# Kernel optimization log

Hardware: AMD Instinct MI355X
Metric: run time of the kernel (lower is better)

The kernel has to match this reference:

```python
import jax, jax.numpy as jnp
import numpy as np

N_NODES = 100000
N_EDGES = 1600000
NFEAT, NHID, NCLASS = 512, 256, 40
ALPHA = 1.0
N_POWERS = 10


def setup_inputs() -> dict:
    key = jax.random.key(0)
    ks = jax.random.split(key, 8)
    x = jax.random.normal(ks[0], (N_NODES, NFEAT), dtype=jnp.float32)
    edge_index = jax.random.randint(ks[1], (2, N_EDGES), 0, N_NODES)
    # Kaiming-ish init, scale = 1/sqrt(fan_in)
    W1 = jax.random.normal(ks[2], (NHID, NFEAT), dtype=jnp.float32) / np.sqrt(NFEAT)
    b1 = jnp.zeros((NHID,), jnp.float32)
    W2 = jax.random.normal(ks[3], (NHID, NHID), dtype=jnp.float32) / np.sqrt(NHID)
    b2 = jnp.zeros((NHID,), jnp.float32)
    W3 = jax.random.normal(ks[4], (NCLASS, NHID), dtype=jnp.float32) / np.sqrt(NHID)
    b3 = jnp.zeros((NCLASS,), jnp.float32)
    return {"x": x, "edge_index": edge_index, "W1": W1, "b1": b1,
            "W2": W2, "b2": b2, "W3": W3, "b3": b3}


def reference(x, edge_index, W1, b1, W2, b2, W3, b3):
    N = x.shape[0]
    # --- build DA-normalized adjacency with self-loops (to_normalized_sparsetensor, mode='DA') ---
    self_loop = jnp.arange(N)
    rows = jnp.concatenate([edge_index[0], self_loop])  # [E+N]
    cols = jnp.concatenate([edge_index[1], self_loop])  # [E+N]
    deg = jax.ops.segment_sum(jnp.ones(rows.shape[0], x.dtype), rows, num_segments=N)
    # DA mode: rows scaled by deg_inv_sqrt^2 == deg^{-1}
    deg_inv = jnp.where(deg > 0, 1.0 / deg, 0.0)
    w = deg_inv[rows]  # per-edge weight, [E+N]

    def spmm(v):  # A @ v, v: [N, C]
        return jax.ops.segment_sum(w[:, None] * v[cols], rows, num_segments=N)

    # --- MLP (dropout=0, eval mode) ---
    h = jax.nn.relu(x @ W1.T + b1)
    h = jax.nn.relu(h @ W2.T + b2)
    h = h @ W3.T + b3  # [N, NCLASS]

    # --- approximate_invphi_x power iteration (beta=0 branch) ---
    c1 = ALPHA / (1.0 + ALPHA)
    c2 = 1.0 / (1.0 + ALPHA)
    invphi = h
    for _ in range(N_POWERS):
        invphi = c1 * spmm(invphi) + c2 * h
    return invphi
```

## Files before the change

kernel.cpp:

```cpp
#include <hip/hip_runtime.h>
#include <type_traits>

#define N_NODES 100000
#define N_EDGES 1600000
#define NFEAT 512
#define NHID 256
#define NCLASS 40
#define NPAD 100096
#define NPAD2 100352

#define NBUCK 196
#define BROWS 512
#define NBLK_BIN 256
#define EPB 6250

#define CDUM 1916000
#define COLN 1916032

#define ZA (N_NODES * 32)
#define ZB (N_NODES * 8)
#define BLK_A 1563
#define BLK_B 391

typedef __bf16 bf16;
typedef __bf16 bf16x8 __attribute__((ext_vector_type(8)));
typedef __bf16 bf16x4 __attribute__((ext_vector_type(4)));
typedef float f32x4 __attribute__((ext_vector_type(4)));
typedef int i32x4 __attribute__((ext_vector_type(4)));


__global__ __launch_bounds__(256) void bin_count(const int* __restrict__ rows,
                                                 int* __restrict__ bcnt) {
    __shared__ int hist[NBUCK];
    int t = threadIdx.x, b = blockIdx.x;
    for (int i = t; i < NBUCK; i += 256) hist[i] = 0;
    __syncthreads();
    int base = b * EPB;
    for (int i = t; i < EPB; i += 256) atomicAdd(&hist[rows[base + i] >> 9], 1);
    __syncthreads();
    for (int i = t; i < NBUCK; i += 256) bcnt[i * NBLK_BIN + b] = hist[i];
}

__global__ __launch_bounds__(256) void bin_scan(const int* __restrict__ bcnt,
                                                int* __restrict__ boff2,
                                                int* __restrict__ btot) {
    __shared__ int sh[256];
    int t = threadIdx.x, bu = blockIdx.x;
    int v = bcnt[bu * 256 + t];
    sh[t] = v;
    __syncthreads();
    for (int off = 1; off < 256; off <<= 1) {
        int x = (t >= off) ? sh[t - off] : 0;
        __syncthreads();
        sh[t] += x;
        __syncthreads();
    }
    boff2[t * NBUCK + bu] = sh[t] - v;
    if (t == 255) btot[bu] = sh[255];
}

__global__ __launch_bounds__(256) void base_scan(const int* __restrict__ btot,
                                                 int* __restrict__ bbase) {
    __shared__ int sh[256];
    int t = threadIdx.x;
    int v = (t < NBUCK) ? btot[t] : 0;
    sh[t] = v;
    __syncthreads();
    for (int off = 1; off < 256; off <<= 1) {
        int x = (t >= off) ? sh[t - off] : 0;
        __syncthreads();
        sh[t] += x;
        __syncthreads();
    }
    if (t < NBUCK) bbase[t] = sh[t] - v;
    if (t == NBUCK - 1) bbase[NBUCK] = sh[t];
}

__global__ __launch_bounds__(256) void bin_scatter(const int* __restrict__ rows,
                                                   const int* __restrict__ cols,
                                                   const int* __restrict__ boff2,
                                                   const int* __restrict__ bbase,
                                                   int* __restrict__ binned) {
    __shared__ int cur[NBUCK];
    int t = threadIdx.x, b = blockIdx.x;
    for (int i = t; i < NBUCK; i += 256) cur[i] = bbase[i] + boff2[b * NBUCK + i];
    __syncthreads();
    int base = b * EPB;
    for (int i = t; i < EPB; i += 256) {
        int r = rows[base + i], c = cols[base + i];
        int pos = atomicAdd(&cur[r >> 9], 1);
        binned[pos] = ((r & 511) << 17) | c;
    }
}

__global__ __launch_bounds__(256) void bucket_csr(const int* __restrict__ binned,
                                                  const int* __restrict__ bbase,
                                                  int2* __restrict__ rowptr2,
                                                  int* __restrict__ colidx,
                                                  float* __restrict__ dinv) {
    __shared__ int cnt[BROWS];
    __shared__ int pref[BROWS];
    __shared__ int psum[256];
    int t = threadIdx.x, bu = blockIdx.x;
    cnt[t] = 0;
    cnt[t + 256] = 0;
    __syncthreads();
    int base = bbase[bu], end = bbase[bu + 1];
    for (int i = base + t; i < end; i += 256) atomicAdd(&cnt[binned[i] >> 17], 1);
    __syncthreads();
    int c0 = cnt[2 * t], c1 = cnt[2 * t + 1];
    int p0 = (c0 + 3) & ~3, p1 = (c1 + 3) & ~3;
    psum[t] = p0 + p1;
    __syncthreads();
    for (int off = 1; off < 256; off <<= 1) {
        int x = (t >= off) ? psum[t - off] : 0;
        __syncthreads();
        psum[t] += x;
        __syncthreads();
    }
    int pex = psum[t] - (p0 + p1);
    pref[2 * t] = pex;
    pref[2 * t + 1] = pex + p0;
    __syncthreads();
    int pbase = (base & ~3) + bu * 1600;
#pragma unroll
    for (int j = 0; j < 2; j++) {
        int idx = t + j * 256;
        int grow = bu * BROWS + idx;
        int rc = cnt[idx];
        int st = pbase + pref[idx];
        int en = st + ((rc + 3) & ~3);
        if (grow < N_NODES) {
            rowptr2[grow] = make_int2(st, en);
            dinv[grow] = 0.5f / (float)(rc + 1);
            for (int k = st + rc; k < en; k++) colidx[k] = N_NODES;
        } else {
            rowptr2[grow] = make_int2(0, 0);
        }
        pref[idx] = st;
    }
    __syncthreads();
    for (int i = base + t; i < end; i += 256) {
        int v = binned[i];
        int pos = atomicAdd(&pref[v >> 17], 1);
        colidx[pos] = v & 0x1FFFF;
    }
}


__global__ void cvt_f2b(const float* __restrict__ a, bf16* __restrict__ b, int n) {
    int i = blockIdx.x * 256 + threadIdx.x;
    if (i < n) b[i] = (bf16)a[i];
}

__global__ void pad_w3(const float* __restrict__ W3, const float* __restrict__ b3,
                       bf16* __restrict__ W3p, float* __restrict__ b3p) {
    int i = blockIdx.x * 256 + threadIdx.x;
    int r = i >> 8;
    W3p[i] = (bf16)((r < NCLASS) ? W3[(size_t)r * 256 + (i & 255)] : 0.f);
    if (i < 64) b3p[i] = (i < NCLASS) ? b3[i] : 0.f;
}

__global__ void zero_dummy(bf16* vAi, bf16* vA0, bf16* vA1,
                           bf16* vBi, bf16* vB0, bf16* vB1,
                           int* colidx) {
    int i = threadIdx.x;
    if (i < 32) {
        vAi[(size_t)ZA + i] = (bf16)0.f;
        vA0[(size_t)ZA + i] = (bf16)0.f;
        vA1[(size_t)ZA + i] = (bf16)0.f;
    }
    if (i < 8) {
        vBi[(size_t)ZB + i] = (bf16)0.f;
        vB0[(size_t)ZB + i] = (bf16)0.f;
        vB1[(size_t)ZB + i] = (bf16)0.f;
        colidx[CDUM + i] = N_NODES;
    }
}


template <int BN, typename AT, bool RELU, int OUTMODE>
__global__ __launch_bounds__(256) void gemm_mfma(const AT* __restrict__ A,
                                                 const bf16* __restrict__ B,
                                                 const float* __restrict__ bias,
                                                 bf16* __restrict__ Cb,
                                                 float* __restrict__ hA,
                                                 float* __restrict__ hB,
                                                 bf16* __restrict__ vA0,
                                                 bf16* __restrict__ vB0,
                                                 int M, int K, int Nout) {
    constexpr int LDT = 40;
    constexpr int WTM = (BN == 128) ? 64 : 32;
    constexpr int MI = WTM / 16;
    constexpr int WMC = 128 / WTM;
    constexpr int BG = BN / 64;
    constexpr bool AF32 = std::is_same<AT, float>::value;
    __shared__ bf16 As[2][128 * LDT];
    __shared__ bf16 Bs[2][BN * LDT];

    int tid = threadIdx.x;
    int wave = tid >> 6, lane = tid & 63;
    int waveM = wave % WMC, waveN = wave / WMC;
    int lc = lane & 15, lq = lane >> 4;

    f32x4 acc[MI][4];
#pragma unroll
    for (int i = 0; i < MI; i++)
#pragma unroll
        for (int j = 0; j < 4; j++) acc[i][j] = (f32x4){0.f, 0.f, 0.f, 0.f};

    int sr = tid >> 2;
    int sc = (tid & 3) * 8;

    float4 paE[2][2], paO[2][2];
    bf16x8 baE[2], baO[2];
    bf16x8 bbE[BG], bbO[BG];

    auto LOAD = [&](int k0, float4 (&pa)[2][2], bf16x8 (&ba)[2], bf16x8 (&bb)[BG]) {
#pragma unroll
        for (int g = 0; g < 2; g++) {
            int grow = blockIdx.y * 128 + sr + g * 64;
            if constexpr (AF32) {
                if (grow < M) {
                    const float* ap = A + (size_t)grow * K + k0 + sc;
                    pa[g][0] = *(const float4*)ap;
                    pa[g][1] = *(const float4*)(ap + 4);
                } else {
                    pa[g][0] = (float4){0.f, 0.f, 0.f, 0.f};
                    pa[g][1] = (float4){0.f, 0.f, 0.f, 0.f};
                }
            } else {
                ba[g] = (grow < M) ? *(const bf16x8*)(A + (size_t)grow * K + k0 + sc)
                                   : (bf16x8){};
            }
        }
#pragma unroll
        for (int g = 0; g < BG; g++) {
            int brow = blockIdx.x * BN + sr + g * 64;
            bb[g] = *(const bf16x8*)(B + (size_t)brow * K + k0 + sc);
        }
    };
    auto STORE = [&](int buf, float4 (&pa)[2][2], bf16x8 (&ba)[2], bf16x8 (&bb)[BG]) {
#pragma unroll
        for (int g = 0; g < 2; g++) {
            bf16x8 val;
            if constexpr (AF32) {
                val[0] = (bf16)pa[g][0].x; val[1] = (bf16)pa[g][0].y;
                val[2] = (bf16)pa[g][0].z; val[3] = (bf16)pa[g][0].w;
                val[4] = (bf16)pa[g][1].x; val[5] = (bf16)pa[g][1].y;
                val[6] = (bf16)pa[g][1].z; val[7] = (bf16)pa[g][1].w;
            } else {
                val = ba[g];
            }
            *(bf16x8*)&As[buf][(sr + g * 64) * LDT + sc] = val;
        }
#pragma unroll
        for (int g = 0; g < BG; g++)
            *(bf16x8*)&Bs[buf][(sr + g * 64) * LDT + sc] = bb[g];
    };
    auto COMPUTE = [&](int cb) {
        bf16x8 af[MI], bfr[4];
#pragma unroll
        for (int i = 0; i < MI; i++)
            af[i] = *(const bf16x8*)&As[cb][(waveM * WTM + i * 16 + lc) * LDT + lq * 8];
#pragma unroll
        for (int j = 0; j < 4; j++)
            bfr[j] = *(const bf16x8*)&Bs[cb][(waveN * 64 + j * 16 + lc) * LDT + lq * 8];
#pragma unroll
        for (int i = 0; i < MI; i++)
#pragma unroll
            for (int j = 0; j < 4; j++)
                acc[i][j] = __builtin_amdgcn_mfma_f32_16x16x32_bf16(af[i], bfr[j], acc[i][j], 0, 0, 0);
    };

    int nt = K / 32;
    LOAD(0, paE, baE, bbE);
    STORE(0, paE, baE, bbE);
    LOAD(32, paE, baE, bbE);
    LOAD(64, paO, baO, bbO);
    __syncthreads();
    for (int t = 0; t < nt; t += 2) {
        STORE(1, paE, baE, bbE);
        if (t + 3 < nt) LOAD((t + 3) * 32, paE, baE, bbE);
        COMPUTE(0);
        __syncthreads();
        if (t + 2 < nt) STORE(0, paO, baO, bbO);
        if (t + 4 < nt) LOAD((t + 4) * 32, paO, baO, bbO);
        COMPUTE(1);
        __syncthreads();
    }

#pragma unroll
    for (int i = 0; i < MI; i++) {
        int row0 = blockIdx.y * 128 + waveM * WTM + i * 16 + lq * 4;
#pragma unroll
        for (int j = 0; j < 4; j++) {
            int colL = waveN * 64 + j * 16 + lc;
            int col = blockIdx.x * BN + colL;
            float bv = bias[col];
#pragma unroll
            for (int reg = 0; reg < 4; reg++) {
                int rr = row0 + reg;
                if (rr < M) {
                    float v = acc[i][j][reg] + bv;
                    if (RELU) v = v > 0.f ? v : 0.f;
                    if (OUTMODE == 0) {
                        Cb[(size_t)rr * Nout + col] = (bf16)v;
                    } else {
                        if (col < 32) {
                            hA[(size_t)rr * 32 + col] = 0.5f * v;
                            vA0[(size_t)rr * 32 + col] = (bf16)v;
                        } else if (col < NCLASS) {
                            hB[(size_t)rr * 8 + (col - 32)] = 0.5f * v;
                            vB0[(size_t)rr * 8 + (col - 32)] = (bf16)v;
                        }
                    }
                }
            }
        }
    }
}


__global__ __launch_bounds__(256) void spmm_split(const bf16* __restrict__ vA,
                                                  const bf16* __restrict__ vB,
                                                  const float* __restrict__ hA,
                                                  const float* __restrict__ hB,
                                                  const int2* __restrict__ rowptr2,
                                                  const int* __restrict__ colidx,
                                                  const float* __restrict__ dinv,
                                                  bf16* __restrict__ oA,
                                                  bf16* __restrict__ oB,
                                                  float* __restrict__ outF,
                                                  int final_it) {
    int b = blockIdx.x;
    int lane = threadIdx.x & 63;
    const int* cdum = colidx + CDUM;
    if (b < BLK_A) {
        int w = b * 4 + (threadIdx.x >> 6);
        int sub = lane & 3;
        int r = w * 16 + (lane >> 2);
        if (r >= N_NODES) return;
        int2 se = rowptr2[r];
        int sx = se.x, d = se.y - se.x;
        int m = d;
#pragma unroll
        for (int off = 4; off < 64; off <<= 1) {
            int x = __shfl_xor(m, off);
            m = m > x ? m : x;
        }
        float4 hv0 = *(const float4*)(hA + (size_t)r * 32 + sub * 8);
        float4 hv1 = *(const float4*)(hA + (size_t)r * 32 + sub * 8 + 4);
        float dv = dinv[r];
        bf16x8 sv = *(const bf16x8*)(vA + (size_t)r * 32 + sub * 8);
        float a[8];
#pragma unroll
        for (int k = 0; k < 8; k++) a[k] = (float)sv[k];
        i32x4 cc = *(const i32x4*)(d > 0 ? colidx + sx : cdum);
        i32x4 cn = *(const i32x4*)(4 < d ? colidx + sx + 4 : cdum);
        bf16x8 G0 = *(const bf16x8*)(vA + (size_t)cc[0] * 32 + sub * 8);
        bf16x8 G1 = *(const bf16x8*)(vA + (size_t)cc[1] * 32 + sub * 8);
        bf16x8 G2 = *(const bf16x8*)(vA + (size_t)cc[2] * 32 + sub * 8);
        bf16x8 G3 = *(const bf16x8*)(vA + (size_t)cc[3] * 32 + sub * 8);
        int m8 = (m + 7) & ~7;
        for (int i = 0; i < m8; i += 8) {
            i32x4 ci8 = *(const i32x4*)((i + 8 < d) ? colidx + sx + i + 8 : cdum);
            bf16x8 H0 = *(const bf16x8*)(vA + (size_t)cn[0] * 32 + sub * 8);
            bf16x8 H1 = *(const bf16x8*)(vA + (size_t)cn[1] * 32 + sub * 8);
            bf16x8 H2 = *(const bf16x8*)(vA + (size_t)cn[2] * 32 + sub * 8);
            bf16x8 H3 = *(const bf16x8*)(vA + (size_t)cn[3] * 32 + sub * 8);
#pragma unroll
            for (int k = 0; k < 8; k++)
                a[k] += ((float)G0[k] + (float)G1[k]) + ((float)G2[k] + (float)G3[k]);
            cn = *(const i32x4*)((i + 12 < d) ? colidx + sx + i + 12 : cdum);
            G0 = *(const bf16x8*)(vA + (size_t)ci8[0] * 32 + sub * 8);
            G1 = *(const bf16x8*)(vA + (size_t)ci8[1] * 32 + sub * 8);
            G2 = *(const bf16x8*)(vA + (size_t)ci8[2] * 32 + sub * 8);
            G3 = *(const bf16x8*)(vA + (size_t)ci8[3] * 32 + sub * 8);
#pragma unroll
            for (int k = 0; k < 8; k++)
                a[k] += ((float)H0[k] + (float)H1[k]) + ((float)H2[k] + (float)H3[k]);
        }
        float res[8];
        res[0] = dv * a[0] + hv0.x; res[1] = dv * a[1] + hv0.y;
        res[2] = dv * a[2] + hv0.z; res[3] = dv * a[3] + hv0.w;
        res[4] = dv * a[4] + hv1.x; res[5] = dv * a[5] + hv1.y;
        res[6] = dv * a[6] + hv1.z; res[7] = dv * a[7] + hv1.w;
        if (final_it) {
            *(float4*)(outF + (size_t)r * NCLASS + sub * 8) = (float4){res[0], res[1], res[2], res[3]};
            *(float4*)(outF + (size_t)r * NCLASS + sub * 8 + 4) = (float4){res[4], res[5], res[6], res[7]};
        } else {
            bf16x8 o;
#pragma unroll
            for (int k = 0; k < 8; k++) o[k] = (bf16)res[k];
            *(bf16x8*)(oA + (size_t)r * 32 + sub * 8) = o;
        }
    } else {
        int w = (b - BLK_A) * 4 + (threadIdx.x >> 6);
        int r = w * 64 + lane;
        int rz = (r < N_NODES) ? r : 0;
        int2 se = rowptr2[r];
        int sx = se.x, d = se.y - se.x;
        int m = d;
#pragma unroll
        for (int off = 1; off < 64; off <<= 1) {
            int x = __shfl_xor(m, off);
            m = m > x ? m : x;
        }
        float4 h0 = *(const float4*)(hB + (size_t)rz * 8);
        float4 h1 = *(const float4*)(hB + (size_t)rz * 8 + 4);
        float dv = dinv[rz];
        bf16x8 sv = *(const bf16x8*)(vB + (size_t)rz * 8);
        float a[8];
#pragma unroll
        for (int k = 0; k < 8; k++) a[k] = (float)sv[k];
        i32x4 cc = *(const i32x4*)(d > 0 ? colidx + sx : cdum);
        i32x4 cn = *(const i32x4*)(4 < d ? colidx + sx + 4 : cdum);
        bf16x8 G0 = *(const bf16x8*)(vB + (size_t)cc[0] * 8);
        bf16x8 G1 = *(const bf16x8*)(vB + (size_t)cc[1] * 8);
        bf16x8 G2 = *(const bf16x8*)(vB + (size_t)cc[2] * 8);
        bf16x8 G3 = *(const bf16x8*)(vB + (size_t)cc[3] * 8);
        int m8 = (m + 7) & ~7;
        for (int i = 0; i < m8; i += 8) {
            i32x4 ci8 = *(const i32x4*)((i + 8 < d) ? colidx + sx + i + 8 : cdum);
            bf16x8 H0 = *(const bf16x8*)(vB + (size_t)cn[0] * 8);
            bf16x8 H1 = *(const bf16x8*)(vB + (size_t)cn[1] * 8);
            bf16x8 H2 = *(const bf16x8*)(vB + (size_t)cn[2] * 8);
            bf16x8 H3 = *(const bf16x8*)(vB + (size_t)cn[3] * 8);
#pragma unroll
            for (int k = 0; k < 8; k++)
                a[k] += ((float)G0[k] + (float)G1[k]) + ((float)G2[k] + (float)G3[k]);
            cn = *(const i32x4*)((i + 12 < d) ? colidx + sx + i + 12 : cdum);
            G0 = *(const bf16x8*)(vB + (size_t)ci8[0] * 8);
            G1 = *(const bf16x8*)(vB + (size_t)ci8[1] * 8);
            G2 = *(const bf16x8*)(vB + (size_t)ci8[2] * 8);
            G3 = *(const bf16x8*)(vB + (size_t)ci8[3] * 8);
#pragma unroll
            for (int k = 0; k < 8; k++)
                a[k] += ((float)H0[k] + (float)H1[k]) + ((float)H2[k] + (float)H3[k]);
        }
        if (r < N_NODES) {
            float res[8];
            res[0] = dv * a[0] + h0.x; res[1] = dv * a[1] + h0.y;
            res[2] = dv * a[2] + h0.z; res[3] = dv * a[3] + h0.w;
            res[4] = dv * a[4] + h1.x; res[5] = dv * a[5] + h1.y;
            res[6] = dv * a[6] + h1.z; res[7] = dv * a[7] + h1.w;
            if (final_it) {
                *(float4*)(outF + (size_t)r * NCLASS + 32) = (float4){res[0], res[1], res[2], res[3]};
                *(float4*)(outF + (size_t)r * NCLASS + 36) = (float4){res[4], res[5], res[6], res[7]};
            } else {
                bf16x8 o;
#pragma unroll
                for (int k = 0; k < 8; k++) o[k] = (bf16)res[k];
                *(bf16x8*)(oB + (size_t)r * 8) = o;
            }
        }
    }
}


extern "C" void kernel_launch(void* const* d_in, const int* in_sizes, int n_in,
                              void* d_out, int out_size, void* d_ws, size_t ws_size,
                              hipStream_t stream) {
    const float* x  = (const float*)d_in[0];
    const int*   ei = (const int*)d_in[1];
    const float* W1 = (const float*)d_in[2];
    const float* b1 = (const float*)d_in[3];
    const float* W2 = (const float*)d_in[4];
    const float* b2 = (const float*)d_in[5];
    const float* W3 = (const float*)d_in[6];
    const float* b3 = (const float*)d_in[7];
    float* out = (float*)d_out;
    const int* rows = ei;
    const int* cols = ei + N_EDGES;

    char* p = (char*)d_ws;
    bf16* hid1 = (bf16*)p;                 p += (size_t)N_NODES * NHID * 2;
    bf16* hid2 = (bf16*)p;                 p += (size_t)N_NODES * NHID * 2;
    float* hA  = (float*)p;                p += (size_t)N_NODES * 32 * 4;
    float* hB  = (float*)p;                p += (size_t)N_NODES * 8 * 4;
    bf16* vAi  = (bf16*)p;                 p += (size_t)(N_NODES + 1) * 32 * 2;
    bf16* vA0  = (bf16*)p;                 p += (size_t)(N_NODES + 1) * 32 * 2;
    bf16* vA1  = (bf16*)p;                 p += (size_t)(N_NODES + 1) * 32 * 2;
    bf16* vBi  = (bf16*)p;                 p += (size_t)(N_NODES + 1) * 8 * 2;
    bf16* vB0  = (bf16*)p;                 p += (size_t)(N_NODES + 1) * 8 * 2;
    bf16* vB1  = (bf16*)p;                 p += (size_t)(N_NODES + 1) * 8 * 2;
    bf16* W1b  = (bf16*)p;                 p += (size_t)NHID * NFEAT * 2;
    bf16* W2b  = (bf16*)p;                 p += (size_t)NHID * NHID * 2;
    bf16* W3p  = (bf16*)p;                 p += (size_t)64 * NHID * 2;
    float* b3p = (float*)p;                p += 64 * 4;
    int* bcnt    = (int*)p;                p += (size_t)NPAD * 4;
    int2* rowptr2 = (int2*)p;              p += (size_t)NPAD2 * 8;
    int* boff2   = (int*)p;                p += (size_t)N_NODES * 4;
    int* colidx  = (int*)p;                p += (size_t)COLN * 4;
    int* bsum    = (int*)p;                p += 512 * 4;
    float* dinv  = (float*)p;              p += (size_t)N_NODES * 4;

    int* btot  = bsum;
    int* bbase = bsum + 256;
    int* binned = (int*)hid1;

    bin_count<<<NBLK_BIN, 256, 0, stream>>>(rows, bcnt);
    bin_scan<<<NBUCK, 256, 0, stream>>>(bcnt, boff2, btot);
    base_scan<<<1, 256, 0, stream>>>(btot, bbase);
    bin_scatter<<<NBLK_BIN, 256, 0, stream>>>(rows, cols, boff2, bbase, binned);
    bucket_csr<<<NBUCK, 256, 0, stream>>>(binned, bbase, rowptr2, colidx, dinv);

    cvt_f2b<<<(NHID * NFEAT + 255) / 256, 256, 0, stream>>>(W1, W1b, NHID * NFEAT);
    cvt_f2b<<<(NHID * NHID + 255) / 256, 256, 0, stream>>>(W2, W2b, NHID * NHID);
    pad_w3<<<(64 * NHID) / 256, 256, 0, stream>>>(W3, b3, W3p, b3p);

    {
        int M = N_NODES;
        int gy = (M + 127) / 128;
        gemm_mfma<128, float, true, 0><<<dim3(2, gy), 256, 0, stream>>>(
            x, W1b, b1, hid1, nullptr, nullptr, nullptr, nullptr, M, NFEAT, NHID);
        gemm_mfma<128, bf16, true, 0><<<dim3(2, gy), 256, 0, stream>>>(
            hid1, W2b, b2, hid2, nullptr, nullptr, nullptr, nullptr, M, NHID, NHID);
        gemm_mfma<64, bf16, false, 1><<<dim3(1, gy), 256, 0, stream>>>(
            hid2, W3p, b3p, nullptr, hA, hB, vAi, vBi, M, NHID, 64);
    }

    zero_dummy<<<1, 64, 0, stream>>>(vAi, vA0, vA1, vBi, vB0, vB1, colidx);

    const bf16* sA = vAi;
    const bf16* sB = vBi;
    for (int it = 0; it < 10; it++) {
        int fin = (it == 9);
        bf16* dA = (it & 1) ? vA1 : vA0;
        bf16* dB = (it & 1) ? vB1 : vB0;
        spmm_split<<<BLK_A + BLK_B, 256, 0, stream>>>(
            sA, sB, hA, hB, rowptr2, colidx, dinv, dA, dB, out, fin);
        sA = dA;
        sB = dB;
    }
}
```

Measured before the change: 805.0 us.

## Split SpMM into separate column-group kernels and relax GEMM barriers and bounds checks

The fused SpMM kernel, which handled both the 32-column and 8-column feature slices in one launch, is split into two kernels. All ten iterations of the A slice now run before all ten of the B slice, so each sequence gathers from a smaller working set that can stay resident in cache. In the GEMM, the full __syncthreads is replaced by a barrier that waits only on LDS traffic, so global prefetch loads stay in flight across the barrier. Row bounds checks become a clamp to the last row. The split doubles the number of kernel launches and gives up running both slices concurrently within one launch.

```diff
diff --git a/kernel.cpp b/kernel.cpp
--- a/kernel.cpp
+++ b/kernel.cpp
@@ -27,6 +27,11 @@
 typedef __bf16 bf16x4 __attribute__((ext_vector_type(4)));
 typedef float f32x4 __attribute__((ext_vector_type(4)));
 typedef int i32x4 __attribute__((ext_vector_type(4)));
+
+__device__ __forceinline__ void barrier_keep_vmem() {
+    asm volatile("s_waitcnt lgkmcnt(0)" ::: "memory");
+    __builtin_amdgcn_s_barrier();
+}
 
 
 __global__ __launch_bounds__(256) void bin_count(const int* __restrict__ rows,
@@ -220,18 +225,13 @@
 #pragma unroll
         for (int g = 0; g < 2; g++) {
             int grow = blockIdx.y * 128 + sr + g * 64;
+            if (grow > M - 1) grow = M - 1;
             if constexpr (AF32) {
-                if (grow < M) {
-                    const float* ap = A + (size_t)grow * K + k0 + sc;
-                    pa[g][0] = *(const float4*)ap;
-                    pa[g][1] = *(const float4*)(ap + 4);
-                } else {
-                    pa[g][0] = (float4){0.f, 0.f, 0.f, 0.f};
-                    pa[g][1] = (float4){0.f, 0.f, 0.f, 0.f};
-                }
+                const float* ap = A + (size_t)grow * K + k0 + sc;
+                pa[g][0] = *(const float4*)ap;
+                pa[g][1] = *(const float4*)(ap + 4);
             } else {
-                ba[g] = (grow < M) ? *(const bf16x8*)(A + (size_t)grow * K + k0 + sc)
-                                   : (bf16x8){};
+                ba[g] = *(const bf16x8*)(A + (size_t)grow * K + k0 + sc);
             }
         }
 #pragma unroll
@@ -278,16 +278,16 @@
     STORE(0, paE, baE, bbE);
     LOAD(32, paE, baE, bbE);
     LOAD(64, paO, baO, bbO);
-    __syncthreads();
+    barrier_keep_vmem();
     for (int t = 0; t < nt; t += 2) {
         STORE(1, paE, baE, bbE);
         if (t + 3 < nt) LOAD((t + 3) * 32, paE, baE, bbE);
         COMPUTE(0);
-        __syncthreads();
+        barrier_keep_vmem();
         if (t + 2 < nt) STORE(0, paO, baO, bbO);
         if (t + 4 < nt) LOAD((t + 4) * 32, paO, baO, bbO);
         COMPUTE(1);
-        __syncthreads();
+        barrier_keep_vmem();
     }
 
 #pragma unroll
@@ -322,138 +322,143 @@
 }
 
 
-__global__ __launch_bounds__(256) void spmm_split(const bf16* __restrict__ vA,
-                                                  const bf16* __restrict__ vB,
-                                                  const float* __restrict__ hA,
-                                                  const float* __restrict__ hB,
-                                                  const int2* __restrict__ rowptr2,
-                                                  const int* __restrict__ colidx,
-                                                  const float* __restrict__ dinv,
-                                                  bf16* __restrict__ oA,
-                                                  bf16* __restrict__ oB,
-                                                  float* __restrict__ outF,
-                                                  int final_it) {
-    int b = blockIdx.x;
+__global__ __launch_bounds__(256) void spmm_A(const bf16* __restrict__ vA,
+                                              const float* __restrict__ hA,
+                                              const int2* __restrict__ rowptr2,
+                                              const int* __restrict__ colidx,
+                                              const float* __restrict__ dinv,
+                                              bf16* __restrict__ oA,
+                                              float* __restrict__ outF,
+                                              int final_it) {
     int lane = threadIdx.x & 63;
     const int* cdum = colidx + CDUM;
-    if (b < BLK_A) {
-        int w = b * 4 + (threadIdx.x >> 6);
-        int sub = lane & 3;
-        int r = w * 16 + (lane >> 2);
-        if (r >= N_NODES) return;
-        int2 se = rowptr2[r];
-        int sx = se.x, d = se.y - se.x;
-        int m = d;
-#pragma unroll
-        for (int off = 4; off < 64; off <<= 1) {
-            int x = __shfl_xor(m, off);
-            m = m > x ? m : x;
-        }
-        float4 hv0 = *(const float4*)(hA + (size_t)r * 32 + sub * 8);
-        float4 hv1 = *(const float4*)(hA + (size_t)r * 32 + sub * 8 + 4);
-        float dv = dinv[r];
-        bf16x8 sv = *(const bf16x8*)(vA + (size_t)r * 32 + sub * 8);
-        float a[8];
-#pragma unroll
-        for (int k = 0; k < 8; k++) a[k] = (float)sv[k];
-        i32x4 cc = *(const i32x4*)(d > 0 ? colidx + sx : cdum);
-        i32x4 cn = *(const i32x4*)(4 < d ? colidx + sx + 4 : cdum);
-        bf16x8 G0 = *(const bf16x8*)(vA + (size_t)cc[0] * 32 + sub * 8);
-        bf16x8 G1 = *(const bf16x8*)(vA + (size_t)cc[1] * 32 + sub * 8);
-        bf16x8 G2 = *(const bf16x8*)(vA + (size_t)cc[2] * 32 + sub * 8);
-        bf16x8 G3 = *(const bf16x8*)(vA + (size_t)cc[3] * 32 + sub * 8);
-        int m8 = (m + 7) & ~7;
-        for (int i = 0; i < m8; i += 8) {
-            i32x4 ci8 = *(const i32x4*)((i + 8 < d) ? colidx + sx + i + 8 : cdum);
-            bf16x8 H0 = *(const bf16x8*)(vA + (size_t)cn[0] * 32 + sub * 8);
-            bf16x8 H1 = *(const bf16x8*)(vA + (size_t)cn[1] * 32 + sub * 8);
-            bf16x8 H2 = *(const bf16x8*)(vA + (size_t)cn[2] * 32 + sub * 8);
-            bf16x8 H3 = *(const bf16x8*)(vA + (size_t)cn[3] * 32 + sub * 8);
-#pragma unroll
-            for (int k = 0; k < 8; k++)
-                a[k] += ((float)G0[k] + (float)G1[k]) + ((float)G2[k] + (float)G3[k]);
-            cn = *(const i32x4*)((i + 12 < d) ? colidx + sx + i + 12 : cdum);
-            G0 = *(const bf16x8*)(vA + (size_t)ci8[0] * 32 + sub * 8);
-            G1 = *(const bf16x8*)(vA + (size_t)ci8[1] * 32 + sub * 8);
-            G2 = *(const bf16x8*)(vA + (size_t)ci8[2] * 32 + sub * 8);
-            G3 = *(const bf16x8*)(vA + (size_t)ci8[3] * 32 + sub * 8);
-#pragma unroll
-            for (int k = 0; k < 8; k++)
-                a[k] += ((float)H0[k] + (float)H1[k]) + ((float)H2[k] + (float)H3[k]);
-        }
+    int w = blockIdx.x * 4 + (threadIdx.x >> 6);
+    int sub = lane & 3;
+    int r = w * 16 + (lane >> 2);
+    if (r >= N_NODES) return;
+    int2 se = rowptr2[r];
+    int sx = se.x, d = se.y - se.x;
+    int m = d;
+#pragma unroll
+    for (int off = 4; off < 64; off <<= 1) {
+        int x = __shfl_xor(m, off);
+        m = m > x ? m : x;
+    }
+    float4 hv0 = *(const float4*)(hA + (size_t)r * 32 + sub * 8);
+    float4 hv1 = *(const float4*)(hA + (size_t)r * 32 + sub * 8 + 4);
+    float dv = dinv[r];
+    bf16x8 sv = *(const bf16x8*)(vA + (size_t)r * 32 + sub * 8);
+    float a[8];
+#pragma unroll
+    for (int k = 0; k < 8; k++) a[k] = (float)sv[k];
+    i32x4 cc = *(const i32x4*)(d > 0 ? colidx + sx : cdum);
+    i32x4 cn = *(const i32x4*)(4 < d ? colidx + sx + 4 : cdum);
+    bf16x8 G0 = *(const bf16x8*)(vA + (size_t)cc[0] * 32 + sub * 8);
+    bf16x8 G1 = *(const bf16x8*)(vA + (size_t)cc[1] * 32 + sub * 8);
+    bf16x8 G2 = *(const bf16x8*)(vA + (size_t)cc[2] * 32 + sub * 8);
+    bf16x8 G3 = *(const bf16x8*)(vA + (size_t)cc[3] * 32 + sub * 8);
+    int m8 = (m + 7) & ~7;
+    for (int i = 0; i < m8; i += 8) {
+        i32x4 ci8 = *(const i32x4*)((i + 8 < d) ? colidx + sx + i + 8 : cdum);
+        bf16x8 H0 = *(const bf16x8*)(vA + (size_t)cn[0] * 32 + sub * 8);
+        bf16x8 H1 = *(const bf16x8*)(vA + (size_t)cn[1] * 32 + sub * 8);
+        bf16x8 H2 = *(const bf16x8*)(vA + (size_t)cn[2] * 32 + sub * 8);
+        bf16x8 H3 = *(const bf16x8*)(vA + (size_t)cn[3] * 32 + sub * 8);
+#pragma unroll
+        for (int k = 0; k < 8; k++)
+            a[k] += ((float)G0[k] + (float)G1[k]) + ((float)G2[k] + (float)G3[k]);
+        cn = *(const i32x4*)((i + 12 < d) ? colidx + sx + i + 12 : cdum);
+        G0 = *(const bf16x8*)(vA + (size_t)ci8[0] * 32 + sub * 8);
+        G1 = *(const bf16x8*)(vA + (size_t)ci8[1] * 32 + sub * 8);
+        G2 = *(const bf16x8*)(vA + (size_t)ci8[2] * 32 + sub * 8);
+        G3 = *(const bf16x8*)(vA + (size_t)ci8[3] * 32 + sub * 8);
+#pragma unroll
+        for (int k = 0; k < 8; k++)
+            a[k] += ((float)H0[k] + (float)H1[k]) + ((float)H2[k] + (float)H3[k]);
+    }
+    float res[8];
+    res[0] = dv * a[0] + hv0.x; res[1] = dv * a[1] + hv0.y;
+    res[2] = dv * a[2] + hv0.z; res[3] = dv * a[3] + hv0.w;
+    res[4] = dv * a[4] + hv1.x; res[5] = dv * a[5] + hv1.y;
+    res[6] = dv * a[6] + hv1.z; res[7] = dv * a[7] + hv1.w;
+    if (final_it) {
+        *(float4*)(outF + (size_t)r * NCLASS + sub * 8) = (float4){res[0], res[1], res[2], res[3]};
+        *(float4*)(outF + (size_t)r * NCLASS + sub * 8 + 4) = (float4){res[4], res[5], res[6], res[7]};
+    } else {
+        bf16x8 o;
+#pragma unroll
+        for (int k = 0; k < 8; k++) o[k] = (bf16)res[k];
+        *(bf16x8*)(oA + (size_t)r * 32 + sub * 8) = o;
+    }
+}
+
+__global__ __launch_bounds__(256) void spmm_B(const bf16* __restrict__ vB,
+                                              const float* __restrict__ hB,
+                                              const int2* __restrict__ rowptr2,
+                                              const int* __restrict__ colidx,
+                                              const float* __restrict__ dinv,
+                                              bf16* __restrict__ oB,
+                                              float* __restrict__ outF,
+                                              int final_it) {
+    int lane = threadIdx.x & 63;
+    const int* cdum = colidx + CDUM;
+    int w = blockIdx.x * 4 + (threadIdx.x >> 6);
+    int r = w * 64 + lane;
+    int rz = (r < N_NODES) ? r : 0;
+    int2 se = rowptr2[r];
+    int sx = se.x, d = se.y - se.x;
+    int m = d;
+#pragma unroll
+    for (int off = 1; off < 64; off <<= 1) {
+        int x = __shfl_xor(m, off);
+        m = m > x ? m : x;
+    }
+    float4 h0 = *(const float4*)(hB + (size_t)rz * 8);
+    float4 h1 = *(const float4*)(hB + (size_t)rz * 8 + 4);
+    float dv = dinv[rz];
+    bf16x8 sv = *(const bf16x8*)(vB + (size_t)rz * 8);
+    float a[8];
+#pragma unroll
+    for (int k = 0; k < 8; k++) a[k] = (float)sv[k];
+    i32x4 cc = *(const i32x4*)(d > 0 ? colidx + sx : cdum);
+    i32x4 cn = *(const i32x4*)(4 < d ? colidx + sx + 4 : cdum);
+    bf16x8 G0 = *(const bf16x8*)(vB + (size_t)cc[0] * 8);
+    bf16x8 G1 = *(const bf16x8*)(vB + (size_t)cc[1] * 8);
+    bf16x8 G2 = *(const bf16x8*)(vB + (size_t)cc[2] * 8);
+    bf16x8 G3 = *(const bf16x8*)(vB + (size_t)cc[3] * 8);
+    int m8 = (m + 7) & ~7;
+    for (int i = 0; i < m8; i += 8) {
+        i32x4 ci8 = *(const i32x4*)((i + 8 < d) ? colidx + sx + i + 8 : cdum);
+        bf16x8 H0 = *(const bf16x8*)(vB + (size_t)cn[0] * 8);
+        bf16x8 H1 = *(const bf16x8*)(vB + (size_t)cn[1] * 8);
+        bf16x8 H2 = *(const bf16x8*)(vB + (size_t)cn[2] * 8);
+        bf16x8 H3 = *(const bf16x8*)(vB + (size_t)cn[3] * 8);
+#pragma unroll
+        for (int k = 0; k < 8; k++)
+            a[k] += ((float)G0[k] + (float)G1[k]) + ((float)G2[k] + (float)G3[k]);
+        cn = *(const i32x4*)((i + 12 < d) ? colidx + sx + i + 12 : cdum);
+        G0 = *(const bf16x8*)(vB + (size_t)ci8[0] * 8);
+        G1 = *(const bf16x8*)(vB + (size_t)ci8[1] * 8);
+        G2 = *(const bf16x8*)(vB + (size_t)ci8[2] * 8);
+        G3 = *(const bf16x8*)(vB + (size_t)ci8[3] * 8);
+#pragma unroll
+        for (int k = 0; k < 8; k++)
+            a[k] += ((float)H0[k] + (float)H1[k]) + ((float)H2[k] + (float)H3[k]);
+    }
+    if (r < N_NODES) {
         float res[8];
-        res[0] = dv * a[0] + hv0.x; res[1] = dv * a[1] + hv0.y;
-        res[2] = dv * a[2] + hv0.z; res[3] = dv * a[3] + hv0.w;
-        res[4] = dv * a[4] + hv1.x; res[5] = dv * a[5] + hv1.y;
-        res[6] = dv * a[6] + hv1.z; res[7] = dv * a[7] + hv1.w;
+        res[0] = dv * a[0] + h0.x; res[1] = dv * a[1] + h0.y;
+        res[2] = dv * a[2] + h0.z; res[3] = dv * a[3] + h0.w;
+        res[4] = dv * a[4] + h1.x; res[5] = dv * a[5] + h1.y;
+        res[6] = dv * a[6] + h1.z; res[7] = dv * a[7] + h1.w;
         if (final_it) {
-            *(float4*)(outF + (size_t)r * NCLASS + sub * 8) = (float4){res[0], res[1], res[2], res[3]};
-            *(float4*)(outF + (size_t)r * NCLASS + sub * 8 + 4) = (float4){res[4], res[5], res[6], res[7]};
+            *(float4*)(outF + (size_t)r * NCLASS + 32) = (float4){res[0], res[1], res[2], res[3]};
+            *(float4*)(outF + (size_t)r * NCLASS + 36) = (float4){res[4], res[5], res[6], res[7]};
         } else {
             bf16x8 o;
 #pragma unroll
             for (int k = 0; k < 8; k++) o[k] = (bf16)res[k];
-            *(bf16x8*)(oA + (size_t)r * 32 + sub * 8) = o;
-        }
-    } else {
-        int w = (b - BLK_A) * 4 + (threadIdx.x >> 6);
-        int r = w * 64 + lane;
-        int rz = (r < N_NODES) ? r : 0;
-        int2 se = rowptr2[r];
-        int sx = se.x, d = se.y - se.x;
-        int m = d;
-#pragma unroll
-        for (int off = 1; off < 64; off <<= 1) {
-            int x = __shfl_xor(m, off);
-            m = m > x ? m : x;
-        }
-        float4 h0 = *(const float4*)(hB + (size_t)rz * 8);
-        float4 h1 = *(const float4*)(hB + (size_t)rz * 8 + 4);
-        float dv = dinv[rz];
-        bf16x8 sv = *(const bf16x8*)(vB + (size_t)rz * 8);
-        float a[8];
-#pragma unroll
-        for (int k = 0; k < 8; k++) a[k] = (float)sv[k];
-        i32x4 cc = *(const i32x4*)(d > 0 ? colidx + sx : cdum);
-        i32x4 cn = *(const i32x4*)(4 < d ? colidx + sx + 4 : cdum);
-        bf16x8 G0 = *(const bf16x8*)(vB + (size_t)cc[0] * 8);
-        bf16x8 G1 = *(const bf16x8*)(vB + (size_t)cc[1] * 8);
-        bf16x8 G2 = *(const bf16x8*)(vB + (size_t)cc[2] * 8);
-        bf16x8 G3 = *(const bf16x8*)(vB + (size_t)cc[3] * 8);
-        int m8 = (m + 7) & ~7;
-        for (int i = 0; i < m8; i += 8) {
-            i32x4 ci8 = *(const i32x4*)((i + 8 < d) ? colidx + sx + i + 8 : cdum);
-            bf16x8 H0 = *(const bf16x8*)(vB + (size_t)cn[0] * 8);
-            bf16x8 H1 = *(const bf16x8*)(vB + (size_t)cn[1] * 8);
-            bf16x8 H2 = *(const bf16x8*)(vB + (size_t)cn[2] * 8);
-            bf16x8 H3 = *(const bf16x8*)(vB + (size_t)cn[3] * 8);
-#pragma unroll
-            for (int k = 0; k < 8; k++)
-                a[k] += ((float)G0[k] + (float)G1[k]) + ((float)G2[k] + (float)G3[k]);
-            cn = *(const i32x4*)((i + 12 < d) ? colidx + sx + i + 12 : cdum);
-            G0 = *(const bf16x8*)(vB + (size_t)ci8[0] * 8);
-            G1 = *(const bf16x8*)(vB + (size_t)ci8[1] * 8);
-            G2 = *(const bf16x8*)(vB + (size_t)ci8[2] * 8);
-            G3 = *(const bf16x8*)(vB + (size_t)ci8[3] * 8);
-#pragma unroll
-            for (int k = 0; k < 8; k++)
-                a[k] += ((float)H0[k] + (float)H1[k]) + ((float)H2[k] + (float)H3[k]);
-        }
-        if (r < N_NODES) {
-            float res[8];
-            res[0] = dv * a[0] + h0.x; res[1] = dv * a[1] + h0.y;
-            res[2] = dv * a[2] + h0.z; res[3] = dv * a[3] + h0.w;
-            res[4] = dv * a[4] + h1.x; res[5] = dv * a[5] + h1.y;
-            res[6] = dv * a[6] + h1.z; res[7] = dv * a[7] + h1.w;
-            if (final_it) {
-                *(float4*)(outF + (size_t)r * NCLASS + 32) = (float4){res[0], res[1], res[2], res[3]};
-                *(float4*)(outF + (size_t)r * NCLASS + 36) = (float4){res[4], res[5], res[6], res[7]};
-            } else {
-                bf16x8 o;
-#pragma unroll
-                for (int k = 0; k < 8; k++) o[k] = (bf16)res[k];
-                *(bf16x8*)(oB + (size_t)r * 8) = o;
-            }
+            *(bf16x8*)(oB + (size_t)r * 8) = o;
         }
     }
 }
@@ -524,14 +529,17 @@
     zero_dummy<<<1, 64, 0, stream>>>(vAi, vA0, vA1, vBi, vB0, vB1, colidx);
 
     const bf16* sA = vAi;
+    for (int it = 0; it < 10; it++) {
+        int fin = (it == 9);
+        bf16* dA = (it & 1) ? vA1 : vA0;
+        spmm_A<<<BLK_A, 256, 0, stream>>>(sA, hA, rowptr2, colidx, dinv, dA, out, fin);
+        sA = dA;
+    }
     const bf16* sB = vBi;
     for (int it = 0; it < 10; it++) {
         int fin = (it == 9);
-        bf16* dA = (it & 1) ? vA1 : vA0;
         bf16* dB = (it & 1) ? vB1 : vB0;
-        spmm_split<<<BLK_A + BLK_B, 256, 0, stream>>>(
-            sA, sB, hA, hB, rowptr2, colidx, dinv, dA, dB, out, fin);
-        sA = dA;
+        spmm_B<<<BLK_B, 256, 0, stream>>>(sB, hB, rowptr2, colidx, dinv, dB, out, fin);
         sB = dB;
     }
 }
```

Measured after the change: 821.6 us. 2.1% more time.

## Bucket rows by degree and process SpMM rows in degree-sorted order

Applied to the files above, without the earlier changes.

Adds a counting sort of nodes by padded degree (histogram, scan, scatter) that builds a permutation, and has the SpMM kernel map each wave's rows through that permutation. Rows in a wave then have similar degree, so the wave-wide max-degree loop does less padded work. The cost is four extra small setup kernels and an indirection that scatters the hA/hB/dinv/output accesses, which lowers coalescing and locality.

```diff
diff --git a/kernel.cpp b/kernel.cpp
--- a/kernel.cpp
+++ b/kernel.cpp
@@ -144,6 +144,54 @@
         int v = binned[i];
         int pos = atomicAdd(&pref[v >> 17], 1);
         colidx[pos] = v & 0x1FFFF;
+    }
+}
+
+
+__global__ void zero_dsort(int* dsort) {
+    if (threadIdx.x < 128) dsort[threadIdx.x] = 0;
+}
+
+__global__ __launch_bounds__(256) void deg_hist(const int2* __restrict__ rowptr2,
+                                                int* __restrict__ dhist) {
+    __shared__ int h[64];
+    int t = threadIdx.x;
+    if (t < 64) h[t] = 0;
+    __syncthreads();
+    int i = blockIdx.x * 256 + t;
+    if (i < N_NODES) {
+        int2 se = rowptr2[i];
+        int bk = (se.y - se.x) >> 2;
+        if (bk > 63) bk = 63;
+        atomicAdd(&h[bk], 1);
+    }
+    __syncthreads();
+    if (t < 64 && h[t]) atomicAdd(&dhist[t], h[t]);
+}
+
+__global__ void deg_scan(const int* __restrict__ dhist, int* __restrict__ dcur) {
+    __shared__ int sh[64];
+    int t = threadIdx.x;
+    sh[t] = dhist[t];
+    __syncthreads();
+    if (t == 0) {
+        int acc = 0;
+        for (int j = 0; j < 64; j++) { int v = sh[j]; sh[j] = acc; acc += v; }
+    }
+    __syncthreads();
+    dcur[t] = sh[t];
+}
+
+__global__ __launch_bounds__(256) void deg_scatter(const int2* __restrict__ rowptr2,
+                                                   int* __restrict__ dcur,
+                                                   int* __restrict__ perm) {
+    int i = blockIdx.x * 256 + threadIdx.x;
+    if (i < N_NODES) {
+        int2 se = rowptr2[i];
+        int bk = (se.y - se.x) >> 2;
+        if (bk > 63) bk = 63;
+        int pos = atomicAdd(&dcur[bk], 1);
+        perm[pos] = i;
     }
 }
 
@@ -329,6 +377,7 @@
                                                   const int2* __restrict__ rowptr2,
                                                   const int* __restrict__ colidx,
                                                   const float* __restrict__ dinv,
+                                                  const int* __restrict__ perm,
                                                   bf16* __restrict__ oA,
                                                   bf16* __restrict__ oB,
                                                   float* __restrict__ outF,
@@ -338,9 +387,10 @@
     const int* cdum = colidx + CDUM;
     if (b < BLK_A) {
         int w = b * 4 + (threadIdx.x >> 6);
+        int idx = w * 16 + (lane >> 2);
+        if (idx >= N_NODES) return;
+        int r = perm[idx];
         int sub = lane & 3;
-        int r = w * 16 + (lane >> 2);
-        if (r >= N_NODES) return;
         int2 se = rowptr2[r];
         int sx = se.x, d = se.y - se.x;
         int m = d;
@@ -397,8 +447,9 @@
         }
     } else {
         int w = (b - BLK_A) * 4 + (threadIdx.x >> 6);
-        int r = w * 64 + lane;
-        int rz = (r < N_NODES) ? r : 0;
+        int idx = w * 64 + lane;
+        int valid = idx < N_NODES;
+        int r = perm[valid ? idx : N_NODES - 1];
         int2 se = rowptr2[r];
         int sx = se.x, d = se.y - se.x;
         int m = d;
@@ -407,10 +458,10 @@
             int x = __shfl_xor(m, off);
             m = m > x ? m : x;
         }
-        float4 h0 = *(const float4*)(hB + (size_t)rz * 8);
-        float4 h1 = *(const float4*)(hB + (size_t)rz * 8 + 4);
-        float dv = dinv[rz];
-        bf16x8 sv = *(const bf16x8*)(vB + (size_t)rz * 8);
+        float4 h0 = *(const float4*)(hB + (size_t)r * 8);
+        float4 h1 = *(const float4*)(hB + (size_t)r * 8 + 4);
+        float dv = dinv[r];
+        bf16x8 sv = *(const bf16x8*)(vB + (size_t)r * 8);
         float a[8];
 #pragma unroll
         for (int k = 0; k < 8; k++) a[k] = (float)sv[k];
@@ -439,7 +490,7 @@
             for (int k = 0; k < 8; k++)
                 a[k] += ((float)H0[k] + (float)H1[k]) + ((float)H2[k] + (float)H3[k]);
         }
-        if (r < N_NODES) {
+        if (valid) {
             float res[8];
             res[0] = dv * a[0] + h0.x; res[1] = dv * a[1] + h0.y;
             res[2] = dv * a[2] + h0.z; res[3] = dv * a[3] + h0.w;
@@ -495,16 +546,25 @@
     int* colidx  = (int*)p;                p += (size_t)COLN * 4;
     int* bsum    = (int*)p;                p += 512 * 4;
     float* dinv  = (float*)p;              p += (size_t)N_NODES * 4;
+    int* dsort   = (int*)p;                p += 128 * 4;
 
     int* btot  = bsum;
     int* bbase = bsum + 256;
     int* binned = (int*)hid1;
+    int* dhist = dsort;
+    int* dcur  = dsort + 64;
+    int* perm  = boff2;
 
     bin_count<<<NBLK_BIN, 256, 0, stream>>>(rows, bcnt);
     bin_scan<<<NBUCK, 256, 0, stream>>>(bcnt, boff2, btot);
     base_scan<<<1, 256, 0, stream>>>(btot, bbase);
     bin_scatter<<<NBLK_BIN, 256, 0, stream>>>(rows, cols, boff2, bbase, binned);
     bucket_csr<<<NBUCK, 256, 0, stream>>>(binned, bbase, rowptr2, colidx, dinv);
+
+    zero_dsort<<<1, 128, 0, stream>>>(dsort);
+    deg_hist<<<(N_NODES + 255) / 256, 256, 0, stream>>>(rowptr2, dhist);
+    deg_scan<<<1, 64, 0, stream>>>(dhist, dcur);
+    deg_scatter<<<(N_NODES + 255) / 256, 256, 0, stream>>>(rowptr2, dcur, perm);
 
     cvt_f2b<<<(NHID * NFEAT + 255) / 256, 256, 0, stream>>>(W1, W1b, NHID * NFEAT);
     cvt_f2b<<<(NHID * NHID + 255) / 256, 256, 0, stream>>>(W2, W2b, NHID * NHID);
@@ -530,7 +590,7 @@
         bf16* dA = (it & 1) ? vA1 : vA0;
         bf16* dB = (it & 1) ? vB1 : vB0;
         spmm_split<<<BLK_A + BLK_B, 256, 0, stream>>>(
-            sA, sB, hA, hB, rowptr2, colidx, dinv, dA, dB, out, fin);
+            sA, sB, hA, hB, rowptr2, colidx, dinv, perm, dA, dB, out, fin);
         sA = dA;
         sB = dB;
     }
```

After: 1.491 ms. +85.3%, slower.
